# Kernel tuning notes

Measured on AMD Instinct MI355X. Metric: run time of the kernel, lower is better.

Reference implementation:

```python
import jax, jax.numpy as jnp
import numpy as np

B_S, SF, N = 16, 4, 192          # pre-stacking batch, stacked_frames, tokens = 256*192/(16*16)
B = B_S * SF                     # 64 rows entering the encoder
D_E, D_P = 768, 384              # d_encoder, d_predictor
NH_E, NH_P = 12, 6
L_E, L_P = 6, 4                  # encoder / predictor depth
FFN = 4
M = 48                           # self.masked_tokens = N // 4 (m_rand fixed to 0 for determinism)
N_AUG = 2
PATCH_DIM = 768                  # 16*16*3
OUT_T = (B_S * M) // B           # 12 tokens per row after the final view


def _ln(x, g, b):
    m = jnp.mean(x, -1, keepdims=True)
    v = jnp.mean((x - m) ** 2, -1, keepdims=True)
    return (x - m) * jax.lax.rsqrt(v + 1e-5) * g + b


def _block(x, ln1g, ln1b, Wqkv, Wo, ln2g, ln2b, W1, W2, nh):
    Bq, T, D = x.shape
    dh = D // nh
    h = _ln(x, ln1g, ln1b)
    q, k, v = jnp.split(h @ Wqkv, 3, axis=-1)
    q = q.reshape(Bq, T, nh, dh).transpose(0, 2, 1, 3)
    k = k.reshape(Bq, T, nh, dh).transpose(0, 2, 1, 3)
    v = v.reshape(Bq, T, nh, dh).transpose(0, 2, 1, 3)
    a = jax.nn.softmax(jnp.einsum('bhqd,bhkd->bhqk', q, k) / jnp.sqrt(jnp.float32(dh)), axis=-1)
    o = jnp.einsum('bhqk,bhkd->bhqd', a, v).transpose(0, 2, 1, 3).reshape(Bq, T, D)
    x = x + o @ Wo
    return x + jax.nn.gelu(_ln(x, ln2g, ln2b) @ W1) @ W2


def _transformer(x, pos, ln1_g, ln1_b, Wqkv, Wo, ln2_g, ln2_b, W1, W2, lnf_g, lnf_b, nh, L):
    x = x + pos[None]
    for i in range(L):
        x = _block(x, ln1_g[i], ln1_b[i], Wqkv[i], Wo[i], ln2_g[i], ln2_b[i], W1[i], W2[i], nh)
    return _ln(x, lnf_g, lnf_b)


def _fwd(X, y, augmentations, mask_pos, proj_W, enc_pos, enc_ln1_g, enc_ln1_b, enc_Wqkv, enc_Wo,
         enc_ln2_g, enc_ln2_b, enc_W1, enc_W2, enc_lnf_g, enc_lnf_b, mask_W, mask_b, mask_emb,
         mm_W0, mm_b0, mm_W, mm_b, pp_W, pp_b, pred_pos, pred_ln1_g, pred_ln1_b, pred_Wqkv,
         pred_Wo, pred_ln2_g, pred_ln2_b, pred_W1, pred_W2, pred_lnf_g, pred_lnf_b):
    Xp = X @ proj_W                                   # encoder.proj (bias=False)
    # ---- get_mask ----
    mpr = jnp.repeat(mask_pos, SF, axis=0)            # (B, M) mask_pos.repeat_interleave(SF, 0)
    row = jnp.repeat(jnp.arange(B_S), SF)             # (B,)
    idx = (mpr + row[:, None] * B_S).reshape(-1)      # faithful to original `* B` arithmetic
    mask = jnp.ones((B, M, 1), Xp.dtype) @ mask_W + mask_b   # MLP(1 -> D_E) on ones
    mask = mask + mask_emb[mpr]                       # positional embedding lookup
    aug = jnp.broadcast_to(jnp.repeat(augmentations, SF, axis=0)[:, None, :], (B, M, N_AUG))
    h = jax.nn.relu(jnp.concatenate([mask, aug], -1)) # mask_mlp: in_act ReLU, 4 linears, out_act ReLU
    h = jax.nn.relu(h @ mm_W0 + mm_b0)
    for i in range(3):
        h = jax.nn.relu(h @ mm_W[i] + mm_b[i])
    Xm = Xp.reshape(B * N, D_E).at[idx].set(h.reshape(-1, D_E)).reshape(B, N, D_E)
    # ---- encoder transformers ----
    Xe = _transformer(Xm, enc_pos, enc_ln1_g, enc_ln1_b, enc_Wqkv, enc_Wo, enc_ln2_g, enc_ln2_b,
                      enc_W1, enc_W2, enc_lnf_g, enc_lnf_b, NH_E, L_E)
    Xq = Xe @ pp_W + pp_b                             # predictor_proj
    Xo = _transformer(Xq, pred_pos, pred_ln1_g, pred_ln1_b, pred_Wqkv, pred_Wo, pred_ln2_g,
                      pred_ln2_b, pred_W1, pred_W2, pred_lnf_g, pred_lnf_b, NH_P, L_P)
    # ---- final gather ----
    mp = jnp.broadcast_to(mask_pos[:, :, None], (B_S, M, D_P)).reshape(B, OUT_T, D_P)
    return jnp.take_along_axis(Xo, mp, axis=1), jnp.take_along_axis(y, mp, axis=1)


def setup_inputs() -> dict:
    key = jax.random.key(0)
    ks = iter(jax.random.split(key, 100))
    nrm = lambda shp, s=0.02: jax.random.normal(next(ks), shp, jnp.float32) * s
    inp = dict(
        X=jax.random.normal(next(ks), (B, N, PATCH_DIM), jnp.float32),
        y=jax.random.normal(next(ks), (B, N, D_P), jnp.float32),
        augmentations=jax.random.uniform(next(ks), (B_S, N_AUG), jnp.float32),
        mask_pos=jax.random.randint(next(ks), (B_S, M), 0, N),
        proj_W=nrm((PATCH_DIM, D_E)),
        enc_pos=nrm((N, D_E)),
        enc_ln1_g=jnp.ones((L_E, D_E)), enc_ln1_b=jnp.zeros((L_E, D_E)),
        enc_Wqkv=nrm((L_E, D_E, 3 * D_E)), enc_Wo=nrm((L_E, D_E, D_E)),
        enc_ln2_g=jnp.ones((L_E, D_E)), enc_ln2_b=jnp.zeros((L_E, D_E)),
        enc_W1=nrm((L_E, D_E, FFN * D_E)), enc_W2=nrm((L_E, FFN * D_E, D_E)),
        enc_lnf_g=jnp.ones((D_E,)), enc_lnf_b=jnp.zeros((D_E,)),
        mask_W=nrm((1, D_E)), mask_b=jnp.zeros((D_E,)),
        mask_emb=nrm((N, D_E)),
        mm_W0=nrm((D_E + N_AUG, D_E)), mm_b0=jnp.zeros((D_E,)),
        mm_W=nrm((3, D_E, D_E)), mm_b=jnp.zeros((3, D_E)),
        pp_W=nrm((D_E, D_P)), pp_b=jnp.zeros((D_P,)),
        pred_pos=nrm((N, D_P)),
        pred_ln1_g=jnp.ones((L_P, D_P)), pred_ln1_b=jnp.zeros((L_P, D_P)),
        pred_Wqkv=nrm((L_P, D_P, 3 * D_P)), pred_Wo=nrm((L_P, D_P, D_P)),
        pred_ln2_g=jnp.ones((L_P, D_P)), pred_ln2_b=jnp.zeros((L_P, D_P)),
        pred_W1=nrm((L_P, D_P, FFN * D_P)), pred_W2=nrm((L_P, FFN * D_P, D_P)),
        pred_lnf_g=jnp.ones((D_P,)), pred_lnf_b=jnp.zeros((D_P,)),
    )
    return inp


def reference(X, y, augmentations, mask_pos, proj_W, enc_pos, enc_ln1_g, enc_ln1_b, enc_Wqkv,
              enc_Wo, enc_ln2_g, enc_ln2_b, enc_W1, enc_W2, enc_lnf_g, enc_lnf_b, mask_W, mask_b,
              mask_emb, mm_W0, mm_b0, mm_W, mm_b, pp_W, pp_b, pred_pos, pred_ln1_g, pred_ln1_b,
              pred_Wqkv, pred_Wo, pred_ln2_g, pred_ln2_b, pred_W1, pred_W2, pred_lnf_g, pred_lnf_b):
    return _fwd(X, y, augmentations, mask_pos, proj_W, enc_pos, enc_ln1_g, enc_ln1_b, enc_Wqkv,
                enc_Wo, enc_ln2_g, enc_ln2_b, enc_W1, enc_W2, enc_lnf_g, enc_lnf_b, mask_W, mask_b,
                mask_emb, mm_W0, mm_b0, mm_W, mm_b, pp_W, pp_b, pred_pos, pred_ln1_g, pred_ln1_b,
                pred_Wqkv, pred_Wo, pred_ln2_g, pred_ln2_b, pred_W1, pred_W2, pred_lnf_g, pred_lnf_b)
```

## Files before the change

kernel.cpp:

```cpp
#include <hip/hip_runtime.h>
#include <hip/hip_bf16.h>
#include <math.h>

typedef __hip_bfloat16 bf16;
typedef __attribute__((ext_vector_type(8))) short bf16x8;
typedef __attribute__((ext_vector_type(4))) float f32x4;
typedef unsigned int u32;

__device__ __forceinline__ float b2f(bf16 v) { return __bfloat162float(v); }
__device__ __forceinline__ bf16 f2b(float v) { return __float2bfloat16(v); }

#define F32MAGIC 0x3F800000u

__device__ __forceinline__ float ldin(const void* p, size_t i, bool f32) {
  return f32 ? ((const float*)p)[i] : b2f(((const bf16*)p)[i]);
}

__device__ __forceinline__ void gload16(const bf16* g, bf16* l) {
  __builtin_amdgcn_global_load_lds((const __attribute__((address_space(1))) u32*)g,
                                   (__attribute__((address_space(3))) u32*)l, 16, 0, 0);
}

__global__ void zf_k(unsigned* p) { if (threadIdx.x == 0) *p = 0u; }

__global__ __launch_bounds__(256) void convert_k(const void* __restrict__ src, int n,
                                                 bf16* __restrict__ dst,
                                                 const unsigned* __restrict__ dflag) {
  bool f32 = (*dflag == F32MAGIC);
  int i = blockIdx.x * 256 + threadIdx.x;
  if (i < n) dst[i] = f2b(ldin(src, (size_t)i, f32));
}

__global__ __launch_bounds__(256) void transpose_k(const void* __restrict__ in,
                                                   bf16* __restrict__ out,
                                                   int K, int N, int Kpad, size_t zelem,
                                                   const unsigned* __restrict__ dflag) {
  bool f32 = (*dflag == F32MAGIC);
  __shared__ bf16 Ts[64][66];
  size_t zin = zelem + (size_t)blockIdx.z * K * N;
  out += (size_t)blockIdx.z * N * Kpad;
  int k0 = blockIdx.x * 64, n0 = blockIdx.y * 64;
  int c = threadIdx.x & 63, r4 = threadIdx.x >> 6;
#pragma unroll
  for (int rr = 0; rr < 16; rr++) {
    int r = rr * 4 + r4;
    int k = k0 + r;
    Ts[r][c] = (k < K) ? f2b(ldin(in, zin + (size_t)k * N + n0 + c, f32)) : f2b(0.f);
  }
  __syncthreads();
#pragma unroll
  for (int rr = 0; rr < 16; rr++) {
    int r = rr * 4 + r4;
    int kk = k0 + c;
    if (kk < Kpad) out[(size_t)(n0 + r) * Kpad + kk] = Ts[c][r];
  }
}

__global__ __launch_bounds__(256) void v0build_k(const int* __restrict__ mask_pos,
                                                 const void* __restrict__ aug,
                                                 const void* __restrict__ mask_W,
                                                 const void* __restrict__ mask_b,
                                                 const void* __restrict__ mask_emb,
                                                 bf16* __restrict__ V0,
                                                 const unsigned* __restrict__ dflag) {
  bool f32 = (*dflag == F32MAGIC);
  int tk = blockIdx.x;
  int s = tk / 48;
  int p = mask_pos[tk];
  for (int d = threadIdx.x; d < 800; d += 256) {
    float v;
    if (d < 768)      v = ldin(mask_W, d, f32) + ldin(mask_b, d, f32) +
                          ldin(mask_emb, (size_t)p * 768 + d, f32);
    else if (d < 770) v = ldin(aug, s * 2 + (d - 768), f32);
    else              v = 0.f;
    V0[(size_t)tk * 800 + d] = f2b(fmaxf(v, 0.f));
  }
}

__global__ __launch_bounds__(256) void scatter_k(const int* __restrict__ mask_pos,
                                                 const bf16* __restrict__ H,
                                                 float* __restrict__ x) {
  int rr = blockIdx.x;
  __shared__ int win;
  if (threadIdx.x == 0) {
    int wfound = -1;
    for (int s = 15; s >= 0 && wfound < 0; s--) {
      int p = rr - 16 * s;
      if (p < 0 || p > 191) continue;
      for (int m = 47; m >= 0; m--)
        if (mask_pos[s * 48 + m] == p) { wfound = s * 48 + m; break; }
    }
    win = wfound;
  }
  __syncthreads();
  if (win >= 0)
    for (int d = threadIdx.x; d < 768; d += 256)
      x[(size_t)rr * 768 + d] = b2f(H[(size_t)win * 768 + d]);
}

__global__ __launch_bounds__(256) void addpos_k(float* __restrict__ x,
                                                const void* __restrict__ pos,
                                                int TD, size_t total,
                                                const unsigned* __restrict__ dflag) {
  bool f32 = (*dflag == F32MAGIC);
  size_t i = (size_t)blockIdx.x * 256 + threadIdx.x;
  if (i < total) x[i] += ldin(pos, i % TD, f32);
}

__global__ __launch_bounds__(256) void ln_k(const float* __restrict__ x,
                                            bf16* __restrict__ out,
                                            const bf16* __restrict__ g,
                                            const bf16* __restrict__ b, int D) {
  int row = blockIdx.x;
  const float* xr = x + (size_t)row * D;
  __shared__ float red1[4], red2[4];
  int tid = threadIdx.x, w = tid >> 6;
  float invD = 1.0f / (float)D;
  float vals[3];
  int nv = 0;
  float s = 0.f;
  for (int d = tid; d < D; d += 256) { float t = xr[d]; vals[nv++] = t; s += t; }
#pragma unroll
  for (int off = 32; off; off >>= 1) s += __shfl_down(s, off);
  if ((tid & 63) == 0) red1[w] = s;
  __syncthreads();
  float mean = (red1[0] + red1[1] + red1[2] + red1[3]) * invD;
  float v = 0.f;
  for (int i = 0; i < nv; i++) { float t = vals[i] - mean; v += t * t; }
#pragma unroll
  for (int off = 32; off; off >>= 1) v += __shfl_down(v, off);
  if ((tid & 63) == 0) red2[w] = v;
  __syncthreads();
  float rstd = rsqrtf((red2[0] + red2[1] + red2[2] + red2[3]) * invD + 1e-5f);
  int i = 0;
  for (int d = tid; d < D; d += 256, i++)
    out[(size_t)row * D + d] = f2b((vals[i] - mean) * rstd * b2f(g[d]) + b2f(b[d]));
}

#define EPI_BIAS   1
#define EPI_RESID  2
#define EPI_GELU   4
#define EPI_RELU   8
#define EPI_OUTF32 16
#define EPI_VSPLIT 32
#define EPI_AINPUT 64

__global__ __launch_bounds__(256) void gemm_bt(const void* __restrict__ A,
                                               const bf16* __restrict__ BT,
                                               void* __restrict__ Cout,
                                               const void* __restrict__ bias,
                                               const float* __restrict__ resid,
                                               bf16* __restrict__ vt,
                                               int M, int N, int K, int epi,
                                               const unsigned* __restrict__ dflag) {
  bool f32 = (*dflag == F32MAGIC);
  bool a_f32 = f32 && (epi & EPI_AINPUT);
  __shared__ __align__(16) bf16 As[128 * 32];
  __shared__ __align__(16) bf16 Bs[128 * 32];
  int tid = threadIdx.x, lane = tid & 63, w = tid >> 6;
  int r = lane & 15, quad = lane >> 4;
  int bm = blockIdx.y * 128, bn = blockIdx.x * 128;
  int wm = (w >> 1) * 64, wn = (w & 1) * 64;
  int srow = lane >> 2, scol = (lane & 3) * 8;
  const bf16* Ab = (const bf16*)A;
  f32x4 acc[4][4];
#pragma unroll
  for (int mi = 0; mi < 4; mi++)
#pragma unroll
    for (int ni = 0; ni < 4; ni++) acc[mi][ni] = (f32x4){0.f, 0.f, 0.f, 0.f};

  for (int kt = 0; kt < K; kt += 32) {
    __syncthreads();
    if (!a_f32) {
#pragma unroll
      for (int i = 0; i < 2; i++) {
        int rb = (w * 2 + i) * 16;
        gload16(Ab + (size_t)(bm + rb + srow) * K + kt + scol, &As[rb * 32]);
        gload16(BT + (size_t)(bn + rb + srow) * K + kt + scol, &Bs[rb * 32]);
      }
    } else {
      const float* Af = (const float*)A;
#pragma unroll
      for (int it = 0; it < 2; it++) {
        int t = tid + it * 256;
        int row = t >> 2, col = (t & 3) * 8;
        size_t aidx = (size_t)(bm + row) * K + kt + col;
        bf16 tmp[8];
#pragma unroll
        for (int j = 0; j < 8; j++) tmp[j] = f2b(Af[aidx + j]);
        *(bf16x8*)&As[row * 32 + col] = *(const bf16x8*)tmp;
        *(bf16x8*)&Bs[row * 32 + col] = *(const bf16x8*)(BT + (size_t)(bn + row) * K + kt + col);
      }
    }
    __syncthreads();
    bf16x8 af[4], bfr[4];
#pragma unroll
    for (int mi = 0; mi < 4; mi++)
      af[mi] = *(const bf16x8*)&As[(wm + mi * 16 + r) * 32 + quad * 8];
#pragma unroll
    for (int ni = 0; ni < 4; ni++)
      bfr[ni] = *(const bf16x8*)&Bs[(wn + ni * 16 + r) * 32 + quad * 8];
#pragma unroll
    for (int mi = 0; mi < 4; mi++)
#pragma unroll
      for (int ni = 0; ni < 4; ni++)
        acc[mi][ni] = __builtin_amdgcn_mfma_f32_16x16x32_bf16(af[mi], bfr[ni], acc[mi][ni], 0, 0, 0);
  }

  int Dm3 = N / 3;
#pragma unroll
  for (int mi = 0; mi < 4; mi++)
#pragma unroll
    for (int ni = 0; ni < 4; ni++)
#pragma unroll
      for (int i = 0; i < 4; i++) {
        int row = bm + wm + mi * 16 + quad * 4 + i;
        int col = bn + wn + ni * 16 + r;
        float v = acc[mi][ni][i];
        if (epi & EPI_BIAS)  v += ldin(bias, col, f32);
        if (epi & EPI_RESID) v += resid[(size_t)row * N + col];
        if (epi & EPI_GELU) {
          float x3 = v * v * v;
          v = 0.5f * v * (1.f + tanhf(0.7978845608f * (v + 0.044715f * x3)));
        }
        if (epi & EPI_RELU) v = fmaxf(v, 0.f);
        if ((epi & EPI_VSPLIT) && col >= 2 * Dm3) {
          int dg = col - 2 * Dm3, hh = dg >> 6, dd = dg & 63;
          int bb = row / 192, tt = row - bb * 192;
          int NHl = Dm3 >> 6;
          vt[((size_t)(bb * NHl + hh) * 64 + dd) * 200 + tt] = f2b(v);
        } else if (epi & EPI_OUTF32) {
          ((float*)Cout)[(size_t)row * N + col] = v;
        } else {
          ((bf16*)Cout)[(size_t)row * N + col] = f2b(v);
        }
      }
}

__global__ __launch_bounds__(256) void attn_k(const bf16* __restrict__ qkv,
                                              const bf16* __restrict__ vt,
                                              bf16* __restrict__ ao,
                                              int D, int NH) {
  const int D3 = 3 * D;
  int pid = blockIdx.x;
  int pan = pid % 3, bh = pid / 3;
  int b = bh / NH, h = bh % NH;
  __shared__ bf16 VtS[12800];
  __shared__ bf16 Sp[12800];
  int tid = threadIdx.x, lane = tid & 63, w = tid >> 6;
  int r = lane & 15, quad = lane >> 4;

  {
    const bf16* src = vt + (size_t)bh * 12800;
    for (int i = tid; i < 1600; i += 256)
      *(bf16x8*)&VtS[i * 8] = *(const bf16x8*)(src + i * 8);
  }

  const bf16* qbase = qkv + ((size_t)(b * 192 + pan * 64 + w * 16 + r)) * D3 + h * 64;
  bf16x8 afq0 = *(const bf16x8*)(qbase + quad * 8);
  bf16x8 afq1 = *(const bf16x8*)(qbase + 32 + quad * 8);

  f32x4 s[12];
#pragma unroll
  for (int ct = 0; ct < 12; ct++) {
    const bf16* kbase = qkv + ((size_t)(b * 192 + ct * 16 + r)) * D3 + D + h * 64;
    bf16x8 bk0 = *(const bf16x8*)(kbase + quad * 8);
    bf16x8 bk1 = *(const bf16x8*)(kbase + 32 + quad * 8);
    f32x4 a = (f32x4){0.f, 0.f, 0.f, 0.f};
    a = __builtin_amdgcn_mfma_f32_16x16x32_bf16(afq0, bk0, a, 0, 0, 0);
    a = __builtin_amdgcn_mfma_f32_16x16x32_bf16(afq1, bk1, a, 0, 0, 0);
    s[ct] = a;
  }

  float mx[4] = {-3e38f, -3e38f, -3e38f, -3e38f};
#pragma unroll
  for (int ct = 0; ct < 12; ct++)
#pragma unroll
    for (int i = 0; i < 4; i++) {
      float sv = s[ct][i] * 0.125f;
      s[ct][i] = sv;
      mx[i] = fmaxf(mx[i], sv);
    }
#pragma unroll
  for (int off = 1; off < 16; off <<= 1)
#pragma unroll
    for (int i = 0; i < 4; i++) mx[i] = fmaxf(mx[i], __shfl_xor(mx[i], off));
  float l[4] = {0.f, 0.f, 0.f, 0.f};
#pragma unroll
  for (int ct = 0; ct < 12; ct++)
#pragma unroll
    for (int i = 0; i < 4; i++) {
      float e = __expf(s[ct][i] - mx[i]);
      s[ct][i] = e;
      l[i] += e;
    }
#pragma unroll
  for (int off = 1; off < 16; off <<= 1)
#pragma unroll
    for (int i = 0; i < 4; i++) l[i] += __shfl_xor(l[i], off);
  float linv[4];
#pragma unroll
  for (int i = 0; i < 4; i++) linv[i] = 1.0f / l[i];

#pragma unroll
  for (int ct = 0; ct < 12; ct++)
#pragma unroll
    for (int i = 0; i < 4; i++)
      Sp[(w * 16 + quad * 4 + i) * 200 + ct * 16 + r] = f2b(s[ct][i]);

  __syncthreads();

  f32x4 o[4];
#pragma unroll
  for (int ct = 0; ct < 4; ct++) o[ct] = (f32x4){0.f, 0.f, 0.f, 0.f};
#pragma unroll
  for (int ks = 0; ks < 6; ks++) {
    bf16x8 ap = *(const bf16x8*)&Sp[(w * 16 + r) * 200 + ks * 32 + quad * 8];
#pragma unroll
    for (int ct = 0; ct < 4; ct++) {
      bf16x8 bv = *(const bf16x8*)&VtS[(ct * 16 + r) * 200 + ks * 32 + quad * 8];
      o[ct] = __builtin_amdgcn_mfma_f32_16x16x32_bf16(ap, bv, o[ct], 0, 0, 0);
    }
  }
  int qg = pan * 64 + w * 16 + quad * 4;
#pragma unroll
  for (int ct = 0; ct < 4; ct++)
#pragma unroll
    for (int i = 0; i < 4; i++)
      ao[((size_t)(b * 192 + qg + i)) * D + h * 64 + ct * 16 + r] = f2b(o[ct][i] * linv[i]);
}

__global__ __launch_bounds__(256) void gather_k(const bf16* __restrict__ Xo,
                                                const void* __restrict__ y,
                                                const int* __restrict__ mask_pos,
                                                void* __restrict__ out,
                                                const unsigned* __restrict__ dflag) {
  bool f32 = (*dflag == F32MAGIC);
  int i = blockIdx.x * 256 + threadIdx.x;
  if (i >= 64 * 12 * 384) return;
  int d = i % 384;
  int bt = i / 384;
  int t = bt % 12, b = bt / 12;
  int p = mask_pos[(b >> 2) * 48 + (b & 3) * 12 + t];
  size_t src = ((size_t)(b * 192 + p)) * 384 + d;
  float o0 = b2f(Xo[src]);
  float o1 = ldin(y, src, f32);
  if (f32) {
    ((float*)out)[i] = o0;
    ((float*)out)[294912 + i] = o1;
  } else {
    ((bf16*)out)[i] = f2b(o0);
    ((bf16*)out)[294912 + i] = f2b(o1);
  }
}

extern "C" void kernel_launch(void* const* d_in, const int* in_sizes, int n_in,
                              void* d_out, int out_size, void* d_ws, size_t ws_size,
                              hipStream_t stream) {
  (void)in_sizes; (void)n_in; (void)out_size; (void)ws_size;
  const void* X          = d_in[0];
  const void* y          = d_in[1];
  const void* aug        = d_in[2];
  const int*  mask_pos   = (const int*)d_in[3];
  const void* proj_W     = d_in[4];
  const void* enc_pos    = d_in[5];
  const void* enc_ln1_g  = d_in[6];
  const void* enc_ln1_b  = d_in[7];
  const void* enc_Wqkv   = d_in[8];
  const void* enc_Wo     = d_in[9];
  const void* enc_ln2_g  = d_in[10];
  const void* enc_ln2_b  = d_in[11];
  const void* enc_W1     = d_in[12];
  const void* enc_W2     = d_in[13];
  const void* enc_lnf_g  = d_in[14];
  const void* enc_lnf_b  = d_in[15];
  const void* mask_W     = d_in[16];
  const void* mask_b     = d_in[17];
  const void* mask_emb   = d_in[18];
  const void* mm_W0      = d_in[19];
  const void* mm_b0      = d_in[20];
  const void* mm_W       = d_in[21];
  const void* mm_b       = d_in[22];
  const void* pp_W       = d_in[23];
  const void* pp_b       = d_in[24];
  const void* pred_pos   = d_in[25];
  const void* pred_ln1_g = d_in[26];
  const void* pred_ln1_b = d_in[27];
  const void* pred_Wqkv  = d_in[28];
  const void* pred_Wo    = d_in[29];
  const void* pred_ln2_g = d_in[30];
  const void* pred_ln2_b = d_in[31];
  const void* pred_W1    = d_in[32];
  const void* pred_W2    = d_in[33];
  const void* pred_lnf_g = d_in[34];
  const void* pred_lnf_b = d_in[35];

  const unsigned* dflag = (const unsigned*)enc_ln1_g;

  size_t off = 0;
  char* base = (char*)d_ws;
  auto alloc = [&](size_t bytes) -> char* {
    char* p = base + off;
    off += (bytes + 255) & ~(size_t)255;
    return p;
  };
  bf16*  arena = (bf16*)alloc((size_t)6144 * 3072 * 2);
  float* xbuf  = (float*)alloc((size_t)12288 * 768 * 4);
  bf16*  hbuf  = (bf16*)alloc((size_t)12288 * 768 * 2);
  bf16*  vtc   = (bf16*)alloc((size_t)384 * 64 * 200 * 2);
  bf16*  wta   = (bf16*)alloc((size_t)3072 * 768 * 2);
  bf16*  wtb   = (bf16*)alloc((size_t)3072 * 768 * 2);
  bf16*  prm   = (bf16*)alloc((size_t)32768 * 2);
  unsigned* zf = (unsigned*)alloc(256);

  bf16* V0 = arena;
  bf16* V1 = arena + (size_t)768 * 800;
  bf16* V2 = V1 + (size_t)768 * 768;
  bf16* Hb = V2 + (size_t)768 * 768;

  const int O_E1G = 0,     O_E1B = 4608,  O_E2G = 9216,  O_E2B = 13824;
  const int O_EFG = 18432, O_EFB = 19200, O_MMB = 19968;
  const int O_P1G = 22272, O_P1B = 23808, O_P2G = 25344, O_P2B = 26880;
  const int O_PFG = 28416, O_PFB = 28800;

  dim3 blk(256);
  const int CM = 6144;

  zf_k<<<1, blk, 0, stream>>>(zf);

  auto stage = [&](const void* src, int n, int o) {
    convert_k<<<dim3((n + 255) / 256), blk, 0, stream>>>(src, n, prm + o, dflag);
  };
  stage(enc_ln1_g, 4608, O_E1G);  stage(enc_ln1_b, 4608, O_E1B);
  stage(enc_ln2_g, 4608, O_E2G);  stage(enc_ln2_b, 4608, O_E2B);
  stage(enc_lnf_g, 768,  O_EFG);  stage(enc_lnf_b, 768,  O_EFB);
  stage(mm_b,      2304, O_MMB);
  stage(pred_ln1_g, 1536, O_P1G); stage(pred_ln1_b, 1536, O_P1B);
  stage(pred_ln2_g, 1536, O_P2G); stage(pred_ln2_b, 1536, O_P2B);
  stage(pred_lnf_g, 384,  O_PFG); stage(pred_lnf_b, 384,  O_PFB);

  v0build_k<<<768, blk, 0, stream>>>(mask_pos, aug, mask_W, mask_b, mask_emb, V0, dflag);
  transpose_k<<<dim3(13, 12, 1), blk, 0, stream>>>(mm_W0, wta, 770, 768, 800, 0, dflag);
  transpose_k<<<dim3(12, 12, 3), blk, 0, stream>>>(mm_W, wtb, 768, 768, 768, 0, dflag);
  gemm_bt<<<dim3(6, 6), blk, 0, stream>>>(V0, wta, V1, mm_b0, nullptr, nullptr,
                                          768, 768, 800, EPI_BIAS | EPI_RELU, dflag);
  gemm_bt<<<dim3(6, 6), blk, 0, stream>>>(V1, wtb, V2, prm + O_MMB, nullptr, nullptr,
                                          768, 768, 768, EPI_BIAS | EPI_RELU, zf);
  gemm_bt<<<dim3(6, 6), blk, 0, stream>>>(V2, wtb + (size_t)768 * 768, V1, prm + O_MMB + 768,
                                          nullptr, nullptr, 768, 768, 768,
                                          EPI_BIAS | EPI_RELU, zf);
  gemm_bt<<<dim3(6, 6), blk, 0, stream>>>(V1, wtb + (size_t)2 * 768 * 768, Hb, prm + O_MMB + 1536,
                                          nullptr, nullptr, 768, 768, 768,
                                          EPI_BIAS | EPI_RELU, zf);

  transpose_k<<<dim3(12, 12, 1), blk, 0, stream>>>(proj_W, wta, 768, 768, 768, 0, dflag);
  gemm_bt<<<dim3(6, 96), blk, 0, stream>>>(X, wta, xbuf, nullptr, nullptr, nullptr,
                                           12288, 768, 768, EPI_OUTF32 | EPI_AINPUT, dflag);
  scatter_k<<<432, blk, 0, stream>>>(mask_pos, Hb, xbuf);
  addpos_k<<<36864, blk, 0, stream>>>(xbuf, enc_pos, 192 * 768, (size_t)12288 * 768, dflag);

  for (int L = 0; L < 6; L++) {
    ln_k<<<12288, blk, 0, stream>>>(xbuf, hbuf, prm + O_E1G + L * 768, prm + O_E1B + L * 768, 768);
    transpose_k<<<dim3(12, 36, 1), blk, 0, stream>>>(enc_Wqkv, wta, 768, 2304, 768,
                                                     (size_t)L * 768 * 2304, dflag);
    for (int c = 0; c < 2; c++) {
      gemm_bt<<<dim3(18, 48), blk, 0, stream>>>(hbuf + (size_t)c * CM * 768, wta, arena,
                                                nullptr, nullptr, vtc, CM, 2304, 768,
                                                EPI_VSPLIT, zf);
      attn_k<<<1152, blk, 0, stream>>>(arena, vtc, hbuf + (size_t)c * CM * 768, 768, 12);
    }
    transpose_k<<<dim3(12, 12, 1), blk, 0, stream>>>(enc_Wo, wta, 768, 768, 768,
                                                     (size_t)L * 768 * 768, dflag);
    gemm_bt<<<dim3(6, 96), blk, 0, stream>>>(hbuf, wta, xbuf, nullptr, xbuf, nullptr,
                                             12288, 768, 768, EPI_RESID | EPI_OUTF32, zf);
    ln_k<<<12288, blk, 0, stream>>>(xbuf, hbuf, prm + O_E2G + L * 768, prm + O_E2B + L * 768, 768);
    transpose_k<<<dim3(12, 48, 1), blk, 0, stream>>>(enc_W1, wta, 768, 3072, 768,
                                                     (size_t)L * 768 * 3072, dflag);
    transpose_k<<<dim3(48, 12, 1), blk, 0, stream>>>(enc_W2, wtb, 3072, 768, 3072,
                                                     (size_t)L * 3072 * 768, dflag);
    for (int c = 0; c < 2; c++) {
      gemm_bt<<<dim3(24, 48), blk, 0, stream>>>(hbuf + (size_t)c * CM * 768, wta, arena,
                                                nullptr, nullptr, nullptr, CM, 3072, 768,
                                                EPI_GELU, zf);
      gemm_bt<<<dim3(6, 48), blk, 0, stream>>>(arena, wtb, xbuf + (size_t)c * CM * 768,
                                               nullptr, xbuf + (size_t)c * CM * 768, nullptr,
                                               CM, 768, 3072, EPI_RESID | EPI_OUTF32, zf);
    }
  }
  ln_k<<<12288, blk, 0, stream>>>(xbuf, hbuf, prm + O_EFG, prm + O_EFB, 768);

  transpose_k<<<dim3(12, 6, 1), blk, 0, stream>>>(pp_W, wta, 768, 384, 768, 0, dflag);
  gemm_bt<<<dim3(3, 96), blk, 0, stream>>>(hbuf, wta, xbuf, pp_b, nullptr, nullptr,
                                           12288, 384, 768, EPI_BIAS | EPI_OUTF32, dflag);
  addpos_k<<<18432, blk, 0, stream>>>(xbuf, pred_pos, 192 * 384, (size_t)12288 * 384, dflag);

  for (int L = 0; L < 4; L++) {
    ln_k<<<12288, blk, 0, stream>>>(xbuf, hbuf, prm + O_P1G + L * 384, prm + O_P1B + L * 384, 384);
    transpose_k<<<dim3(6, 18, 1), blk, 0, stream>>>(pred_Wqkv, wta, 384, 1152, 384,
                                                    (size_t)L * 384 * 1152, dflag);
    for (int c = 0; c < 2; c++) {
      gemm_bt<<<dim3(9, 48), blk, 0, stream>>>(hbuf + (size_t)c * CM * 384, wta, arena,
                                               nullptr, nullptr, vtc, CM, 1152, 384,
                                               EPI_VSPLIT, zf);
      attn_k<<<576, blk, 0, stream>>>(arena, vtc, hbuf + (size_t)c * CM * 384, 384, 6);
    }
    transpose_k<<<dim3(6, 6, 1), blk, 0, stream>>>(pred_Wo, wta, 384, 384, 384,
                                                   (size_t)L * 384 * 384, dflag);
    gemm_bt<<<dim3(3, 96), blk, 0, stream>>>(hbuf, wta, xbuf, nullptr, xbuf, nullptr,
                                             12288, 384, 384, EPI_RESID | EPI_OUTF32, zf);
    ln_k<<<12288, blk, 0, stream>>>(xbuf, hbuf, prm + O_P2G + L * 384, prm + O_P2B + L * 384, 384);
    transpose_k<<<dim3(6, 24, 1), blk, 0, stream>>>(pred_W1, wta, 384, 1536, 384,
                                                    (size_t)L * 384 * 1536, dflag);
    transpose_k<<<dim3(24, 6, 1), blk, 0, stream>>>(pred_W2, wtb, 1536, 384, 1536,
                                                    (size_t)L * 1536 * 384, dflag);
    for (int c = 0; c < 2; c++) {
      gemm_bt<<<dim3(12, 48), blk, 0, stream>>>(hbuf + (size_t)c * CM * 384, wta, arena,
                                                nullptr, nullptr, nullptr, CM, 1536, 384,
                                                EPI_GELU, zf);
      gemm_bt<<<dim3(3, 48), blk, 0, stream>>>(arena, wtb, xbuf + (size_t)c * CM * 384,
                                               nullptr, xbuf + (size_t)c * CM * 384, nullptr,
                                               CM, 384, 1536, EPI_RESID | EPI_OUTF32, zf);
    }
  }
  ln_k<<<12288, blk, 0, stream>>>(xbuf, hbuf, prm + O_PFG, prm + O_PFB, 384);

  gather_k<<<1152, blk, 0, stream>>>(hbuf, y, mask_pos, d_out, dflag);
}
```

Before: 5.823 ms.

## Double-buffer GEMM LDS tiles, add XCD-aware block swizzle, pre-convert input X

The GEMM kernel now double-buffers its shared-memory A/B tiles, so the global-to-LDS copy of the next K-slice is issued before the MFMAs on the current slice run, and it keeps one barrier per iteration. Block indices are remapped so that consecutive tiles are grouped per XCD, which is meant to improve L2 locality across the chiplets. The f32-input path in the GEMM is removed: X is converted to bf16 by a separate kernel into arena scratch, so the projection GEMM can use the direct LDS-load path. In exchange, LDS use doubles, and an extra conversion pass over X plus a scratch region inside the arena are added.

```diff
diff --git a/kernel.cpp b/kernel.cpp
--- a/kernel.cpp
+++ b/kernel.cpp
@@ -143,9 +143,8 @@
 #define EPI_RELU   8
 #define EPI_OUTF32 16
 #define EPI_VSPLIT 32
-#define EPI_AINPUT 64
-
-__global__ __launch_bounds__(256) void gemm_bt(const void* __restrict__ A,
+
+__global__ __launch_bounds__(256) void gemm_bt(const bf16* __restrict__ A,
                                                const bf16* __restrict__ BT,
                                                void* __restrict__ Cout,
                                                const void* __restrict__ bias,
@@ -154,57 +153,64 @@
                                                int M, int N, int K, int epi,
                                                const unsigned* __restrict__ dflag) {
   bool f32 = (*dflag == F32MAGIC);
-  bool a_f32 = f32 && (epi & EPI_AINPUT);
-  __shared__ __align__(16) bf16 As[128 * 32];
-  __shared__ __align__(16) bf16 Bs[128 * 32];
+  __shared__ __align__(16) bf16 As[2][128 * 32];
+  __shared__ __align__(16) bf16 Bs[2][128 * 32];
   int tid = threadIdx.x, lane = tid & 63, w = tid >> 6;
   int r = lane & 15, quad = lane >> 4;
-  int bm = blockIdx.y * 128, bn = blockIdx.x * 128;
+
+  int nbx = gridDim.x;
+  int nwg = nbx * (int)gridDim.y;
+  int orig = blockIdx.y * nbx + blockIdx.x;
+  int q8 = nwg >> 3, r8 = nwg & 7;
+  int xcd = orig & 7, idx = orig >> 3;
+  int swz = (xcd < r8 ? xcd * (q8 + 1) : r8 * (q8 + 1) + (xcd - r8) * q8) + idx;
+  int bm = (swz / nbx) * 128, bn = (swz % nbx) * 128;
+
   int wm = (w >> 1) * 64, wn = (w & 1) * 64;
   int srow = lane >> 2, scol = (lane & 3) * 8;
-  const bf16* Ab = (const bf16*)A;
   f32x4 acc[4][4];
 #pragma unroll
   for (int mi = 0; mi < 4; mi++)
 #pragma unroll
     for (int ni = 0; ni < 4; ni++) acc[mi][ni] = (f32x4){0.f, 0.f, 0.f, 0.f};
 
-  for (int kt = 0; kt < K; kt += 32) {
-    __syncthreads();
-    if (!a_f32) {
-#pragma unroll
-      for (int i = 0; i < 2; i++) {
-        int rb = (w * 2 + i) * 16;
-        gload16(Ab + (size_t)(bm + rb + srow) * K + kt + scol, &As[rb * 32]);
-        gload16(BT + (size_t)(bn + rb + srow) * K + kt + scol, &Bs[rb * 32]);
-      }
-    } else {
-      const float* Af = (const float*)A;
-#pragma unroll
-      for (int it = 0; it < 2; it++) {
-        int t = tid + it * 256;
-        int row = t >> 2, col = (t & 3) * 8;
-        size_t aidx = (size_t)(bm + row) * K + kt + col;
-        bf16 tmp[8];
-#pragma unroll
-        for (int j = 0; j < 8; j++) tmp[j] = f2b(Af[aidx + j]);
-        *(bf16x8*)&As[row * 32 + col] = *(const bf16x8*)tmp;
-        *(bf16x8*)&Bs[row * 32 + col] = *(const bf16x8*)(BT + (size_t)(bn + row) * K + kt + col);
-      }
-    }
-    __syncthreads();
+  int nt = K >> 5;
+  auto stage = [&](int t, int b) {
+    int kt = t << 5;
+#pragma unroll
+    for (int i = 0; i < 2; i++) {
+      int rb = (w * 2 + i) * 16;
+      gload16(A + (size_t)(bm + rb + srow) * K + kt + scol, &As[b][rb * 32]);
+      gload16(BT + (size_t)(bn + rb + srow) * K + kt + scol, &Bs[b][rb * 32]);
+    }
+  };
+
+  stage(0, 0);
+  asm volatile("s_waitcnt vmcnt(0)" ::: "memory");
+  __builtin_amdgcn_s_barrier();
+  __builtin_amdgcn_sched_barrier(0);
+
+  int cur = 0;
+  for (int t = 0; t < nt; t++) {
+    if (t + 1 < nt) stage(t + 1, cur ^ 1);
     bf16x8 af[4], bfr[4];
 #pragma unroll
     for (int mi = 0; mi < 4; mi++)
-      af[mi] = *(const bf16x8*)&As[(wm + mi * 16 + r) * 32 + quad * 8];
+      af[mi] = *(const bf16x8*)&As[cur][(wm + mi * 16 + r) * 32 + quad * 8];
 #pragma unroll
     for (int ni = 0; ni < 4; ni++)
-      bfr[ni] = *(const bf16x8*)&Bs[(wn + ni * 16 + r) * 32 + quad * 8];
+      bfr[ni] = *(const bf16x8*)&Bs[cur][(wn + ni * 16 + r) * 32 + quad * 8];
 #pragma unroll
     for (int mi = 0; mi < 4; mi++)
 #pragma unroll
       for (int ni = 0; ni < 4; ni++)
         acc[mi][ni] = __builtin_amdgcn_mfma_f32_16x16x32_bf16(af[mi], bfr[ni], acc[mi][ni], 0, 0, 0);
+    if (t + 1 < nt) {
+      asm volatile("s_waitcnt vmcnt(0)" ::: "memory");
+      __builtin_amdgcn_s_barrier();
+      __builtin_amdgcn_sched_barrier(0);
+      cur ^= 1;
+    }
   }
 
   int Dm3 = N / 3;
@@ -417,6 +423,7 @@
   bf16* V1 = arena + (size_t)768 * 800;
   bf16* V2 = V1 + (size_t)768 * 768;
   bf16* Hb = V2 + (size_t)768 * 768;
+  bf16* Xb = arena + (size_t)4 * 1024 * 1024;
 
   const int O_E1G = 0,     O_E1B = 4608,  O_E2G = 9216,  O_E2B = 13824;
   const int O_EFG = 18432, O_EFB = 19200, O_MMB = 19968;
@@ -438,6 +445,8 @@
   stage(pred_ln1_g, 1536, O_P1G); stage(pred_ln1_b, 1536, O_P1B);
   stage(pred_ln2_g, 1536, O_P2G); stage(pred_ln2_b, 1536, O_P2B);
   stage(pred_lnf_g, 384,  O_PFG); stage(pred_lnf_b, 384,  O_PFB);
+
+  convert_k<<<dim3(36864), blk, 0, stream>>>(X, 12288 * 768, Xb, dflag);
 
   v0build_k<<<768, blk, 0, stream>>>(mask_pos, aug, mask_W, mask_b, mask_emb, V0, dflag);
   transpose_k<<<dim3(13, 12, 1), blk, 0, stream>>>(mm_W0, wta, 770, 768, 800, 0, dflag);
@@ -454,8 +463,8 @@
                                           EPI_BIAS | EPI_RELU, zf);
 
   transpose_k<<<dim3(12, 12, 1), blk, 0, stream>>>(proj_W, wta, 768, 768, 768, 0, dflag);
-  gemm_bt<<<dim3(6, 96), blk, 0, stream>>>(X, wta, xbuf, nullptr, nullptr, nullptr,
-                                           12288, 768, 768, EPI_OUTF32 | EPI_AINPUT, dflag);
+  gemm_bt<<<dim3(6, 96), blk, 0, stream>>>(Xb, wta, xbuf, nullptr, nullptr, nullptr,
+                                           12288, 768, 768, EPI_OUTF32, zf);
   scatter_k<<<432, blk, 0, stream>>>(mask_pos, Hb, xbuf);
   addpos_k<<<36864, blk, 0, stream>>>(xbuf, enc_pos, 192 * 768, (size_t)12288 * 768, dflag);
 
```

Result: faster. 5.547 ms (-4.7%).
